# Kernel optimization log

Measured on AMD Instinct MI355X. Metric: run time of the kernel, lower is better.

The kernel has to match this reference:

```python
import jax, jax.numpy as jnp
import numpy as np

# Config from init_kwargs
B = 16
CIN = 128
COUT = 256
N = 16        # num_filters
L = 32        # length
K = 3         # kernel_size
KAPPA = 4
STRIDE = 1
PAD = 2
LP = L + PAD  # padded spatial length for FFT


def make_wn():
    # DFT-derived channel-mixing matrix, (cin, d) with d = cout // n
    v = np.arange(CIN)[:, None]
    sr = N * CIN // COUT
    inds = np.arange(CIN)[np.arange(CIN) % sr == 0]
    M = v @ v[inds].T  # (cin, d)
    wn = np.exp((2j * np.pi / CIN) * M) / CIN
    return jnp.asarray(wn.astype(np.complex64))


def setup_inputs() -> dict:
    key = jax.random.key(0)
    k1, k2 = jax.random.split(key)
    x = jax.random.normal(k1, (B, CIN, L, L), dtype=jnp.float32)
    rng = float(np.sqrt(KAPPA / (CIN * K * K)))
    weight = (jax.random.uniform(k2, (N, CIN // KAPPA, K, K), dtype=jnp.float32) - 0.5) * 2.0 * rng
    return {"x": x, "weight": weight}


def reference(x, weight):
    wn = make_wn()  # complex64 (CIN, COUT//N), constant buffer
    # 3D real FFT over (channel, h, w); weight zero-padded from cin//kappa -> cin channels
    x_hat = jnp.fft.rfftn(x, s=(CIN, LP, LP), axes=(-3, -2, -1))          # (B, CIN, LP, LP//2+1)
    w_hat = jnp.fft.rfftn(weight, s=(CIN, LP, LP), axes=(-3, -2, -1))     # (N, CIN, LP, LP//2+1)
    freq = jnp.einsum('bchw,nchw->bnchw', x_hat, w_hat)                   # broadcast, no reduction
    out = jnp.fft.irfftn(freq, s=(LP, LP), axes=(-2, -1))                 # real (B, N, CIN, LP, LP)
    # complex channel mix contracting c -> d; result complex, take real part
    out = jnp.einsum('cd,bnchw->bndhw', wn, out)                          # (B, N, D, LP, LP) complex
    out = out.real[:, :, :, PAD:, PAD:]                                   # (B, N, D, L, L)
    out = jnp.transpose(out, (0, 2, 1, 3, 4))                             # (B, D, N, L, L)
    out = out.reshape(out.shape[0], -1, out.shape[3], out.shape[4])       # (B, COUT, L, L)
    if STRIDE == 2:
        idx = jnp.arange(0, L, 2)
        out = out[:, :, idx, :][:, :, :, idx]
    return out
```

## Files before the change

kernel.cpp:

```cpp
#include <hip/hip_runtime.h>
#include <hip/hip_bf16.h>


typedef __attribute__((ext_vector_type(8))) short short8;
typedef __attribute__((ext_vector_type(4))) float floatx4;

#define NT 256
#define SROW 35
#define SOCT (10 * SROW)

static __device__ __forceinline__ short bf16bits(float f) {
    __hip_bfloat16 h = __float2bfloat16(f);
    return __builtin_bit_cast(short, h);
}

__global__ __launch_bounds__(NT, 4)
void fconv_mfma(const float* __restrict__ x,
                const float* __restrict__ wgt,
                float* __restrict__ out) {
    __shared__ __align__(16) short xs[4 * SOCT * 8];
    __shared__ __align__(16) short wf[9 * 640];

    const int quarter = blockIdx.x;
    const int d       = blockIdx.y;
    const int b       = blockIdx.z;
    const int r0      = quarter * 8;
    const int tid     = threadIdx.x;
    const int dup     = ((d & 7) == 0);

    const float* xb_base = x + ((size_t)b << 17);

#pragma unroll
    for (int pp = 0; pp < 2; ++pp) {
        const int p  = tid + pp * NT;
        const int n  = p >> 5;
        const int c2 = p & 31;
        const float* wb = wgt + (size_t)(n * 32 + c2) * 9;
#pragma unroll
        for (int k = 0; k < 9; ++k)
            wf[(8 - k) * 640 + n * 40 + c2] = bf16bits(wb[k]);
    }

    {
        const int oct = tid >> 6;
        const int rem = tid & 63;
        const int sq  = rem >> 3;
        const int r   = rem & 7;
        const int gr  = r0 + r;
        short8 g[4];
        if (gr < 32) {
            const float* base = xb_base + (gr << 5) + (sq << 2);
            float vals[8][4];
#pragma unroll
            for (int j = 0; j < 8; ++j) {
                const int c2  = oct * 8 + j;
                const int c1a = (8 * d - c2) & 127;
                float4 A = *(const float4*)(base + (c1a << 10));
                if (!dup) {
                    const int c1b = (-8 * d - c2) & 127;
                    const float4 B = *(const float4*)(base + (c1b << 10));
                    A.x = 0.5f * (A.x + B.x); A.y = 0.5f * (A.y + B.y);
                    A.z = 0.5f * (A.z + B.z); A.w = 0.5f * (A.w + B.w);
                }
                vals[j][0] = A.x; vals[j][1] = A.y;
                vals[j][2] = A.z; vals[j][3] = A.w;
            }
#pragma unroll
            for (int ss = 0; ss < 4; ++ss)
#pragma unroll
                for (int j = 0; j < 8; ++j) g[ss][j] = bf16bits(vals[j][ss]);
        } else {
#pragma unroll
            for (int ss = 0; ss < 4; ++ss)
#pragma unroll
                for (int j = 0; j < 8; ++j) g[ss][j] = 0;
        }
#pragma unroll
        for (int ss = 0; ss < 4; ++ss)
            *(short8*)&xs[(oct * SOCT + r * SROW + (sq << 2) + ss) << 3] = g[ss];
    }
    if (tid < 64) {
        const int oct = tid >> 4;
        const int rem = tid & 15;
        const int sq  = rem >> 1;
        const int r   = 8 + (rem & 1);
        const int gr  = r0 + r;
        short8 g[4];
        if (gr < 32) {
            const float* base = xb_base + (gr << 5) + (sq << 2);
            float vals[8][4];
#pragma unroll
            for (int j = 0; j < 8; ++j) {
                const int c2  = oct * 8 + j;
                const int c1a = (8 * d - c2) & 127;
                float4 A = *(const float4*)(base + (c1a << 10));
                if (!dup) {
                    const int c1b = (-8 * d - c2) & 127;
                    const float4 B = *(const float4*)(base + (c1b << 10));
                    A.x = 0.5f * (A.x + B.x); A.y = 0.5f * (A.y + B.y);
                    A.z = 0.5f * (A.z + B.z); A.w = 0.5f * (A.w + B.w);
                }
                vals[j][0] = A.x; vals[j][1] = A.y;
                vals[j][2] = A.z; vals[j][3] = A.w;
            }
#pragma unroll
            for (int ss = 0; ss < 4; ++ss)
#pragma unroll
                for (int j = 0; j < 8; ++j) g[ss][j] = bf16bits(vals[j][ss]);
        } else {
#pragma unroll
            for (int ss = 0; ss < 4; ++ss)
#pragma unroll
                for (int j = 0; j < 8; ++j) g[ss][j] = 0;
        }
#pragma unroll
        for (int ss = 0; ss < 4; ++ss)
            *(short8*)&xs[(oct * SOCT + r * SROW + (sq << 2) + ss) << 3] = g[ss];
    }
    if (tid < 80) {
        const int oct = tid / 20;
        const int rem = tid - oct * 20;
        const int r   = rem >> 1;
        const int s   = 32 + (rem & 1);
        short8 z = {0, 0, 0, 0, 0, 0, 0, 0};
        *(short8*)&xs[(oct * SOCT + r * SROW + s) << 3] = z;
    }

    __syncthreads();

    const int lane = tid & 63;
    const int c    = lane & 15;
    const int q    = lane >> 4;
    short8 af[9];
#pragma unroll
    for (int t = 0; t < 9; ++t)
        af[t] = *(const short8*)&wf[t * 640 + c * 40 + q * 8];

    const int w = tid >> 6;
#pragma unroll
    for (int i = 0; i < 4; ++i) {
        const int lr = 2 * w + (i >> 1);
        const int s0 = (i & 1) << 4;
        floatx4 acc = {0.f, 0.f, 0.f, 0.f};
        const short* basep = &xs[(q * SOCT + lr * SROW + s0 + c) << 3];
#pragma unroll
        for (int u = 0; u < 3; ++u)
#pragma unroll
            for (int v = 0; v < 3; ++v) {
                const short8 bf = *(const short8*)(basep + ((u * SROW + v) << 3));
                acc = __builtin_amdgcn_mfma_f32_16x16x32_bf16(af[u * 3 + v], bf, acc, 0, 0, 0);
            }
        float* op = out + (size_t)(((b * 256 + d * 16 + q * 4) * 32 + (r0 + lr)) * 32 + s0 + c);
        op[0]    = acc.x;
        op[1024] = acc.y;
        op[2048] = acc.z;
        op[3072] = acc.w;
        if (d >= 1 && d <= 7) {
            float* op2 = out + (size_t)(((b * 256 + (16 - d) * 16 + q * 4) * 32 + (r0 + lr)) * 32 + s0 + c);
            op2[0]    = acc.x;
            op2[1024] = acc.y;
            op2[2048] = acc.z;
            op2[3072] = acc.w;
        }
    }
}

extern "C" void kernel_launch(void* const* d_in, const int* in_sizes, int n_in,
                              void* d_out, int out_size, void* d_ws, size_t ws_size,
                              hipStream_t stream) {
    const float* x   = (const float*)d_in[0];
    const float* wgt = (const float*)d_in[1];
    float* out = (float*)d_out;
    (void)in_sizes; (void)n_in; (void)out_size; (void)d_ws; (void)ws_size;

    dim3 grid(4, 9, 16);
    fconv_mfma<<<grid, dim3(NT), 0, stream>>>(x, wgt, out);
}
```

Baseline: 76.02 us.

## Split output rows into 4-row bands to double grid and raise occupancy

Each block now computes 4 output rows instead of 8, so the grid doubles from 4 to 8 row bands, and launch bounds are raised to 6 blocks per CU. The smaller band shrinks the LDS x tile from 10 to 6 rows and folds the staging loads into one pass over 192 threads. The bf16 conversion now packs pairs into bfloat162 values. The halo rows are loaded proportionally more often, adding redundant global reads and weight staging per block in exchange for more parallelism.

```diff
diff --git a/kernel.cpp b/kernel.cpp
--- a/kernel.cpp
+++ b/kernel.cpp
@@ -7,26 +7,21 @@
 
 #define NT 256
 #define SROW 35
-#define SOCT (10 * SROW)
+#define SOCT (6 * SROW)
 
-static __device__ __forceinline__ short bf16bits(float f) {
-    __hip_bfloat16 h = __float2bfloat16(f);
-    return __builtin_bit_cast(short, h);
-}
-
-__global__ __launch_bounds__(NT, 4)
+__global__ __launch_bounds__(NT, 6)
 void fconv_mfma(const float* __restrict__ x,
                 const float* __restrict__ wgt,
                 float* __restrict__ out) {
     __shared__ __align__(16) short xs[4 * SOCT * 8];
     __shared__ __align__(16) short wf[9 * 640];
 
-    const int quarter = blockIdx.x;
-    const int d       = blockIdx.y;
-    const int b       = blockIdx.z;
-    const int r0      = quarter * 8;
-    const int tid     = threadIdx.x;
-    const int dup     = ((d & 7) == 0);
+    const int band = blockIdx.x;
+    const int d    = blockIdx.y;
+    const int b    = blockIdx.z;
+    const int r0   = band * 4;
+    const int tid  = threadIdx.x;
+    const int dup  = ((d & 7) == 0);
 
     const float* xb_base = x + ((size_t)b << 17);
 
@@ -37,15 +32,17 @@
         const int c2 = p & 31;
         const float* wb = wgt + (size_t)(n * 32 + c2) * 9;
 #pragma unroll
-        for (int k = 0; k < 9; ++k)
-            wf[(8 - k) * 640 + n * 40 + c2] = bf16bits(wb[k]);
+        for (int k = 0; k < 9; ++k) {
+            __hip_bfloat16 h = __float2bfloat16(wb[k]);
+            wf[(8 - k) * 640 + n * 40 + c2] = __builtin_bit_cast(short, h);
+        }
     }
 
-    {
-        const int oct = tid >> 6;
-        const int rem = tid & 63;
-        const int sq  = rem >> 3;
-        const int r   = rem & 7;
+    if (tid < 192) {
+        const int oct = tid / 48;
+        const int rem = tid - oct * 48;
+        const int sq  = rem / 6;
+        const int r   = rem - sq * 6;
         const int gr  = r0 + r;
         short8 g[4];
         if (gr < 32) {
@@ -66,9 +63,14 @@
                 vals[j][2] = A.z; vals[j][3] = A.w;
             }
 #pragma unroll
-            for (int ss = 0; ss < 4; ++ss)
+            for (int ss = 0; ss < 4; ++ss) {
+                union { __hip_bfloat162 h2[4]; short8 s8; } u;
 #pragma unroll
-                for (int j = 0; j < 8; ++j) g[ss][j] = bf16bits(vals[j][ss]);
+                for (int jj = 0; jj < 4; ++jj)
+                    u.h2[jj] = __float22bfloat162_rn(
+                        make_float2(vals[2 * jj][ss], vals[2 * jj + 1][ss]));
+                g[ss] = u.s8;
+            }
         } else {
 #pragma unroll
             for (int ss = 0; ss < 4; ++ss)
@@ -79,47 +81,9 @@
         for (int ss = 0; ss < 4; ++ss)
             *(short8*)&xs[(oct * SOCT + r * SROW + (sq << 2) + ss) << 3] = g[ss];
     }
-    if (tid < 64) {
-        const int oct = tid >> 4;
-        const int rem = tid & 15;
-        const int sq  = rem >> 1;
-        const int r   = 8 + (rem & 1);
-        const int gr  = r0 + r;
-        short8 g[4];
-        if (gr < 32) {
-            const float* base = xb_base + (gr << 5) + (sq << 2);
-            float vals[8][4];
-#pragma unroll
-            for (int j = 0; j < 8; ++j) {
-                const int c2  = oct * 8 + j;
-                const int c1a = (8 * d - c2) & 127;
-                float4 A = *(const float4*)(base + (c1a << 10));
-                if (!dup) {
-                    const int c1b = (-8 * d - c2) & 127;
-                    const float4 B = *(const float4*)(base + (c1b << 10));
-                    A.x = 0.5f * (A.x + B.x); A.y = 0.5f * (A.y + B.y);
-                    A.z = 0.5f * (A.z + B.z); A.w = 0.5f * (A.w + B.w);
-                }
-                vals[j][0] = A.x; vals[j][1] = A.y;
-                vals[j][2] = A.z; vals[j][3] = A.w;
-            }
-#pragma unroll
-            for (int ss = 0; ss < 4; ++ss)
-#pragma unroll
-                for (int j = 0; j < 8; ++j) g[ss][j] = bf16bits(vals[j][ss]);
-        } else {
-#pragma unroll
-            for (int ss = 0; ss < 4; ++ss)
-#pragma unroll
-                for (int j = 0; j < 8; ++j) g[ss][j] = 0;
-        }
-#pragma unroll
-        for (int ss = 0; ss < 4; ++ss)
-            *(short8*)&xs[(oct * SOCT + r * SROW + (sq << 2) + ss) << 3] = g[ss];
-    }
-    if (tid < 80) {
-        const int oct = tid / 20;
-        const int rem = tid - oct * 20;
+    if (tid < 48) {
+        const int oct = tid / 12;
+        const int rem = tid - oct * 12;
         const int r   = rem >> 1;
         const int s   = 32 + (rem & 1);
         short8 z = {0, 0, 0, 0, 0, 0, 0, 0};
@@ -138,11 +102,10 @@
 
     const int w = tid >> 6;
 #pragma unroll
-    for (int i = 0; i < 4; ++i) {
-        const int lr = 2 * w + (i >> 1);
-        const int s0 = (i & 1) << 4;
+    for (int i = 0; i < 2; ++i) {
+        const int s0 = i << 4;
         floatx4 acc = {0.f, 0.f, 0.f, 0.f};
-        const short* basep = &xs[(q * SOCT + lr * SROW + s0 + c) << 3];
+        const short* basep = &xs[(q * SOCT + w * SROW + s0 + c) << 3];
 #pragma unroll
         for (int u = 0; u < 3; ++u)
 #pragma unroll
@@ -150,13 +113,13 @@
                 const short8 bf = *(const short8*)(basep + ((u * SROW + v) << 3));
                 acc = __builtin_amdgcn_mfma_f32_16x16x32_bf16(af[u * 3 + v], bf, acc, 0, 0, 0);
             }
-        float* op = out + (size_t)(((b * 256 + d * 16 + q * 4) * 32 + (r0 + lr)) * 32 + s0 + c);
+        float* op = out + (size_t)(((b * 256 + d * 16 + q * 4) * 32 + (r0 + w)) * 32 + s0 + c);
         op[0]    = acc.x;
         op[1024] = acc.y;
         op[2048] = acc.z;
         op[3072] = acc.w;
         if (d >= 1 && d <= 7) {
-            float* op2 = out + (size_t)(((b * 256 + (16 - d) * 16 + q * 4) * 32 + (r0 + lr)) * 32 + s0 + c);
+            float* op2 = op + (size_t)(16 - 2 * d) * 16384;
             op2[0]    = acc.x;
             op2[1024] = acc.y;
             op2[2048] = acc.z;
@@ -173,6 +136,6 @@
     float* out = (float*)d_out;
     (void)in_sizes; (void)n_in; (void)out_size; (void)d_ws; (void)ws_size;
 
-    dim3 grid(4, 9, 16);
+    dim3 grid(8, 9, 16);
     fconv_mfma<<<grid, dim3(NT), 0, stream>>>(x, wgt, out);
 }
```

Measured after the change: 71.94 us. 1.06x faster.
